# Kernel optimization log

Measured on AMD Instinct MI355X. Metric: run time of the kernel, lower is better.

Reference implementation:

```python
import jax, jax.numpy as jnp
import numpy as np

N = 50000   # nodes
E = 600000  # directed edges
B = 128     # graphs
IN = 128
H = 128
K = 30      # sort-pool k
C_OUT = 32
KER = 5
OUT_DIM = 10
L_OUT = K - KER + 1  # 26


def setup_inputs() -> dict:
    key = jax.random.key(0)
    ks = jax.random.split(key, 12)
    s = 0.05
    return {
        "x": jax.random.normal(ks[0], (N, IN), jnp.float32),
        "edge_index": jax.random.randint(ks[1], (2, E), 0, N),
        "batch": jnp.sort(jax.random.randint(ks[2], (N,), 0, B)),
        "W0": jax.random.normal(ks[3], (IN, H), jnp.float32) * s,
        "b0": jnp.zeros((H,), jnp.float32),
        "W1": jax.random.normal(ks[4], (H, H), jnp.float32) * s,
        "b1": jnp.zeros((H,), jnp.float32),
        "W2": jax.random.normal(ks[5], (H, H), jnp.float32) * s,
        "b2": jnp.zeros((H,), jnp.float32),
        "conv_w": jax.random.normal(ks[6], (C_OUT, H, KER), jnp.float32) * s,
        "conv_b": jnp.zeros((C_OUT,), jnp.float32),
        "lin1_w": jax.random.normal(ks[7], (C_OUT * L_OUT, H), jnp.float32) * s,
        "lin1_b": jnp.zeros((H,), jnp.float32),
        "lin2_w": jax.random.normal(ks[8], (H, OUT_DIM), jnp.float32) * s,
        "lin2_b": jnp.zeros((OUT_DIM,), jnp.float32),
    }


def reference(x, edge_index, batch, W0, b0, W1, b1, W2, b2,
              conv_w, conv_b, lin1_w, lin1_b, lin2_w, lin2_b):
    # --- GCN normalization (A + I, symmetric deg^-1/2) ---
    loops = jnp.arange(N)
    row = jnp.concatenate([edge_index[0], loops])  # source
    col = jnp.concatenate([edge_index[1], loops])  # target (aggregation side)
    deg = jax.ops.segment_sum(jnp.ones_like(col, dtype=x.dtype), col, num_segments=N)
    dinv = jax.lax.rsqrt(jnp.maximum(deg, 1.0))
    norm = dinv[row] * dinv[col]  # [E+N]

    def gcn(h, W, b):
        hw = h @ W                                            # [N,H]
        msg = hw[row] * norm[:, None]                         # gather [E+N,H]
        return jax.ops.segment_sum(msg, col, num_segments=N) + b

    h = jax.nn.relu(gcn(x, W0, b0))
    h = jax.nn.relu(gcn(h, W1, b1))
    h = jax.nn.relu(gcn(h, W2, b2))

    # --- SortAggregation: per-graph sort by last channel (desc), top-K, zero-pad ---
    last = h[:, -1]
    order = jnp.lexsort((-last, batch))  # primary: batch, secondary: last desc
    hs = h[order]
    bs = batch[order]
    counts = jax.ops.segment_sum(jnp.ones((N,), jnp.int32), batch, num_segments=B)
    starts = jnp.cumsum(counts) - counts  # exclusive prefix sum
    rank = jnp.arange(N) - starts[bs]     # within-graph rank after sort
    r = jnp.where(rank < K, rank, K)      # overflow bucket K is discarded
    pooled = jnp.zeros((B, K + 1, H), h.dtype).at[bs, r].add(hs)[:, :K]  # [B,K,H]

    # --- conv1d head (NCH layout, matches torch view/transpose) ---
    xc = jnp.transpose(pooled, (0, 2, 1))  # [B,H,K]
    y = jax.lax.conv_general_dilated(xc, conv_w, (1,), "VALID",
                                     dimension_numbers=("NCH", "OIH", "NCH"))
    y = jax.nn.relu(y + conv_b[None, :, None])  # [B,C_OUT,L_OUT]
    y = y.reshape(B, -1)
    y = jax.nn.relu(y @ lin1_w + lin1_b)
    return y @ lin2_w + lin2_b  # [B,OUT_DIM]
```

## Files before the change

### kernel.cpp

```cpp
#include <hip/hip_runtime.h>
#include <math.h>

#define Nn 50000
#define Ee 600000
#define Bg 128
#define Hd 128
#define Kt 30
#define CO 32
#define KW 5
#define LOUT 26
#define CAP 2048
#define SCB 196
#define MMB 782

typedef float v2f __attribute__((ext_vector_type(2)));
typedef short bf16x8 __attribute__((ext_vector_type(8)));
typedef float f32x4 __attribute__((ext_vector_type(4)));

__device__ __forceinline__ unsigned short bfr(float v) {
    unsigned u = __builtin_bit_cast(unsigned, v);
    unsigned r = (u + 0x7FFFu + ((u >> 16) & 1u)) >> 16;
    return (unsigned short)r;
}
__device__ __forceinline__ float bff(unsigned short h) {
    unsigned u = ((unsigned)h) << 16;
    return __builtin_bit_cast(float, u);
}

__global__ void countpack_kernel(const int* __restrict__ ei, const int* __restrict__ batch,
                            int* __restrict__ deg_i, int* __restrict__ bstart,
                            const float* __restrict__ conv_w, float* __restrict__ wT2,
                            const float* __restrict__ W0, const float* __restrict__ W1,
                            const float* __restrict__ W2,
                            ushort* __restrict__ Bph, ushort* __restrict__ Bpm,
                            ushort* __restrict__ Bpl) {
    int i = blockIdx.x * 256 + threadIdx.x;
    if (i < Ee) atomicAdd(&deg_i[ei[Ee + i]], 1);
    if (i < Nn) {
        int b = batch[i];
        if (i == 0) bstart[b] = 0;
        else if (batch[i - 1] != b) bstart[b] = i;
    }
    if (i == 0) bstart[Bg] = Nn;
    if (i < CO * KW * Hd) {
        int ci = i & 127;
        int r = i >> 7;
        int o = r / KW, k = r - o * KW;
        wT2[i] = conv_w[((size_t)o * Hd + ci) * KW + k];
    }
    if (i < 3 * 2048) {
        int l = i >> 11;
        int r = i & 2047;
        int kc = r >> 9;
        int n = (r >> 6) & 7;
        int lane = r & 63;
        int m = lane & 15, kq = lane >> 4;
        const float* W = (l == 0) ? W0 : (l == 1) ? W1 : W2;
        int col = n * 16 + m;
        size_t off = ((size_t)l * 2048 + (size_t)((kc * 8 + n) * 64 + lane)) * 8;
#pragma unroll
        for (int j = 0; j < 8; ++j) {
            float v = W[(size_t)(kc * 32 + kq * 8 + j) * Hd + col];
            unsigned short h = bfr(v);
            float r1 = v - bff(h);
            unsigned short mid = bfr(r1);
            Bph[off + j] = h;
            Bpm[off + j] = mid;
            Bpl[off + j] = bfr(r1 - bff(mid));
        }
    }
}

__global__ __launch_bounds__(256) void scanBC2_kernel(const int* __restrict__ deg_i,
                            int* __restrict__ row_ptr, float* __restrict__ dinv,
                            int* __restrict__ bstart) {
    __shared__ int ls[256];
    __shared__ int boffS;
    int tid = threadIdx.x;
    int b = blockIdx.x;
    int s = 0;
    for (int k = 0; k < b; ++k)
        s += deg_i[k * 256 + tid] + 1;
    ls[tid] = s;
    __syncthreads();
    for (int off = 128; off > 0; off >>= 1) {
        if (tid < off) ls[tid] += ls[tid + off];
        __syncthreads();
    }
    if (tid == 0) boffS = ls[0];
    __syncthreads();
    int boff = boffS;
    int i = b * 256 + tid;
    int v2 = 0;
    if (i < Nn) {
        int raw = deg_i[i];
        v2 = raw + 1;
        dinv[i] = 1.0f / sqrtf((float)(raw + 2));
    }
    ls[tid] = v2;
    __syncthreads();
    for (int off = 1; off < 256; off <<= 1) {
        int t = (tid >= off) ? ls[tid - off] : 0;
        __syncthreads();
        ls[tid] += t;
        __syncthreads();
    }
    if (i < Nn) row_ptr[i + 1] = ls[tid] + boff;
    if (i == 0) row_ptr[0] = 0;
    if (b == 0 && tid == 0) {
        for (int bb = Bg - 1; bb >= 0; --bb)
            if (bstart[bb] == -1) bstart[bb] = bstart[bb + 1];
    }
}

__device__ __forceinline__ void mmx_body(int bid, int tid,
                            const float* __restrict__ Hin,
                            const ushort* __restrict__ Bph, const ushort* __restrict__ Bpm,
                            const ushort* __restrict__ Bpl,
                            const float* __restrict__ dinv, float* __restrict__ hw,
                            float* __restrict__ col127) {
    __shared__ __align__(16) float At[64][132];
    int w = tid >> 6, lane = tid & 63;
    int m = lane & 15, kq = lane >> 4;
    {
        const f32x4* g4 = (const f32x4*)(Hin + (size_t)bid * 64 * Hd);
        int rowsLeft = Nn - bid * 64;
#pragma unroll
        for (int i = 0; i < 8; ++i) {
            int f = i * 256 + tid;
            int r = f >> 5, c4 = f & 31;
            f32x4 v = (f32x4)0.f;
            if (r < rowsLeft) v = g4[f];
            *(f32x4*)&At[r][c4 * 4] = v;
        }
    }
    __syncthreads();
    const float* arow = &At[w * 16 + m][0];
    f32x4 acc[8];
#pragma unroll
    for (int n = 0; n < 8; ++n) acc[n] = (f32x4)0.f;
#pragma unroll
    for (int kc = 0; kc < 4; ++kc) {
        bf16x8 a0, a1, a2;
        float av[8];
        *(f32x4*)&av[0] = *(const f32x4*)(arow + kc * 32 + kq * 8);
        *(f32x4*)&av[4] = *(const f32x4*)(arow + kc * 32 + kq * 8 + 4);
#pragma unroll
        for (int j = 0; j < 8; ++j) {
            unsigned short h = bfr(av[j]);
            float r1 = av[j] - bff(h);
            unsigned short mid = bfr(r1);
            a0[j] = (short)h;
            a1[j] = (short)mid;
            a2[j] = (short)bfr(r1 - bff(mid));
        }
        const ushort* bhp = Bph + (size_t)((kc * 8) * 64 + lane) * 8;
        const ushort* bmp = Bpm + (size_t)((kc * 8) * 64 + lane) * 8;
        const ushort* blp = Bpl + (size_t)((kc * 8) * 64 + lane) * 8;
#pragma unroll
        for (int n = 0; n < 8; ++n) {
            bf16x8 b0 = *(const bf16x8*)(bhp + (size_t)n * 64 * 8);
            bf16x8 b1 = *(const bf16x8*)(bmp + (size_t)n * 64 * 8);
            bf16x8 b2 = *(const bf16x8*)(blp + (size_t)n * 64 * 8);
            acc[n] = __builtin_amdgcn_mfma_f32_16x16x32_bf16(a0, b0, acc[n], 0, 0, 0);
            acc[n] = __builtin_amdgcn_mfma_f32_16x16x32_bf16(a1, b0, acc[n], 0, 0, 0);
            acc[n] = __builtin_amdgcn_mfma_f32_16x16x32_bf16(a0, b1, acc[n], 0, 0, 0);
            acc[n] = __builtin_amdgcn_mfma_f32_16x16x32_bf16(a1, b1, acc[n], 0, 0, 0);
            acc[n] = __builtin_amdgcn_mfma_f32_16x16x32_bf16(a2, b0, acc[n], 0, 0, 0);
            acc[n] = __builtin_amdgcn_mfma_f32_16x16x32_bf16(a0, b2, acc[n], 0, 0, 0);
        }
    }
    int rbase = bid * 64 + w * 16 + kq * 4;
#pragma unroll
    for (int reg = 0; reg < 4; ++reg) {
        int r = rbase + reg;
        if (r < Nn) {
            float s = dinv[r];
#pragma unroll
            for (int n = 0; n < 8; ++n)
                hw[(size_t)r * Hd + n * 16 + m] = acc[n][reg] * s;
            if (m == 15) col127[r] = acc[7][reg] * s;
        }
    }
}

__global__ __launch_bounds__(256) void mmx_kernel(const float* __restrict__ Hin,
                            const ushort* __restrict__ Bph, const ushort* __restrict__ Bpm,
                            const ushort* __restrict__ Bpl,
                            const float* __restrict__ dinv, float* __restrict__ hw,
                            float* __restrict__ col127) {
    mmx_body(blockIdx.x, threadIdx.x, Hin, Bph, Bpm, Bpl, dinv, hw, col127);
}

__global__ __launch_bounds__(256) void mmxfill_kernel(const float* __restrict__ Hin,
                            const ushort* __restrict__ Bph, const ushort* __restrict__ Bpm,
                            const ushort* __restrict__ Bpl,
                            const float* __restrict__ dinv, float* __restrict__ hw,
                            float* __restrict__ col127,
                            const int* __restrict__ ei, const int* __restrict__ row_ptr,
                            int* __restrict__ cnt, int* __restrict__ csr_src) {
    if (blockIdx.x < MMB) {
        mmx_body(blockIdx.x, threadIdx.x, Hin, Bph, Bpm, Bpl, dinv, hw, col127);
    } else {
        int e = (blockIdx.x - MMB) * 256 + threadIdx.x;
        if (e < Ee) {
            int c = ei[Ee + e];
            int r = ei[e];
            int p = row_ptr[c] + atomicAdd(&cnt[c], 1) + 1;
            csr_src[p] = r;
        }
    }
}

__global__ __launch_bounds__(256) void agg_kernel(const float* __restrict__ hw,
                            const int* __restrict__ row_ptr, const int* __restrict__ csr_src,
                            const float* __restrict__ dinv, const float* __restrict__ bias,
                            float* __restrict__ hout) {
    int node = blockIdx.x * 4 + (threadIdx.x >> 6);
    if (node >= Nn) return;
    int lane = threadIdx.x & 63;
    const v2f* hw2 = (const v2f*)hw;
    v2f a0 = hw2[(size_t)node * 64 + lane];
    v2f a1 = 0.f, a2 = 0.f, a3 = 0.f;
    v2f a4 = 0.f, a5 = 0.f, a6 = 0.f, a7 = 0.f;
    int e0 = row_ptr[node], e1 = row_ptr[node + 1];
    int e = e0;
    for (; e + 7 < e1; e += 8) {
        int s0 = __builtin_nontemporal_load(csr_src + e);
        int s1 = __builtin_nontemporal_load(csr_src + e + 1);
        int s2 = __builtin_nontemporal_load(csr_src + e + 2);
        int s3 = __builtin_nontemporal_load(csr_src + e + 3);
        int s4 = __builtin_nontemporal_load(csr_src + e + 4);
        int s5 = __builtin_nontemporal_load(csr_src + e + 5);
        int s6 = __builtin_nontemporal_load(csr_src + e + 6);
        int s7 = __builtin_nontemporal_load(csr_src + e + 7);
        a0 += hw2[(size_t)s0 * 64 + lane];
        a1 += hw2[(size_t)s1 * 64 + lane];
        a2 += hw2[(size_t)s2 * 64 + lane];
        a3 += hw2[(size_t)s3 * 64 + lane];
        a4 += hw2[(size_t)s4 * 64 + lane];
        a5 += hw2[(size_t)s5 * 64 + lane];
        a6 += hw2[(size_t)s6 * 64 + lane];
        a7 += hw2[(size_t)s7 * 64 + lane];
    }
    if (e + 3 < e1) {
        int s0 = __builtin_nontemporal_load(csr_src + e);
        int s1 = __builtin_nontemporal_load(csr_src + e + 1);
        int s2 = __builtin_nontemporal_load(csr_src + e + 2);
        int s3 = __builtin_nontemporal_load(csr_src + e + 3);
        a4 += hw2[(size_t)s0 * 64 + lane];
        a5 += hw2[(size_t)s1 * 64 + lane];
        a6 += hw2[(size_t)s2 * 64 + lane];
        a7 += hw2[(size_t)s3 * 64 + lane];
        e += 4;
    }
    for (; e < e1; ++e) {
        int s0 = __builtin_nontemporal_load(csr_src + e);
        a0 += hw2[(size_t)s0 * 64 + lane];
    }
    v2f acc = ((a0 + a1) + (a2 + a3)) + ((a4 + a5) + (a6 + a7));
    float d = dinv[node];
    v2f bv = ((const v2f*)bias)[lane];
    v2f o;
    o.x = fmaxf(fmaf(d, acc.x, bv.x), 0.f);
    o.y = fmaxf(fmaf(d, acc.y, bv.y), 0.f);
    ((v2f*)hout)[(size_t)node * 64 + lane] = o;
}

__global__ __launch_bounds__(1024) void tail_kernel(const float* __restrict__ hw,
                            const float* __restrict__ hw127,
                            const int* __restrict__ bstart, const int* __restrict__ row_ptr,
                            const int* __restrict__ csr_src, const float* __restrict__ dinv,
                            const float* __restrict__ b2,
                            const float* __restrict__ wT2, const float* __restrict__ conv_b,
                            const float* __restrict__ l1w, const float* __restrict__ l1b,
                            const float* __restrict__ l2w, const float* __restrict__ l2b,
                            float* __restrict__ out) {
    __shared__ float vals[CAP];
    __shared__ float xcl[Kt][130];
    __shared__ float fl[CO * LOUT];
    __shared__ float pz[8][Hd];
    __shared__ float z[Hd];
    __shared__ int selS[Kt];
    int b = blockIdx.x, tid = threadIdx.x;

    int s0 = bstart[b], s1 = bstart[b + 1];
    int n = s1 - s0;
    int nc = n < CAP ? n : CAP;
    if (tid < Kt) selS[tid] = -1;
    float b2l = b2[127];
    for (int j = tid; j < nc; j += 1024) {
        int node = s0 + j;
        float a0 = hw127[node];
        float a1 = 0.f, a2 = 0.f, a3 = 0.f, a4 = 0.f, a5 = 0.f, a6 = 0.f, a7 = 0.f;
        int e0 = row_ptr[node], e1 = row_ptr[node + 1];
        int e = e0;
        for (; e + 7 < e1; e += 8) {
            int q0 = __builtin_nontemporal_load(csr_src + e);
            int q1 = __builtin_nontemporal_load(csr_src + e + 1);
            int q2 = __builtin_nontemporal_load(csr_src + e + 2);
            int q3 = __builtin_nontemporal_load(csr_src + e + 3);
            int q4 = __builtin_nontemporal_load(csr_src + e + 4);
            int q5 = __builtin_nontemporal_load(csr_src + e + 5);
            int q6 = __builtin_nontemporal_load(csr_src + e + 6);
            int q7 = __builtin_nontemporal_load(csr_src + e + 7);
            a0 += hw127[q0];
            a1 += hw127[q1];
            a2 += hw127[q2];
            a3 += hw127[q3];
            a4 += hw127[q4];
            a5 += hw127[q5];
            a6 += hw127[q6];
            a7 += hw127[q7];
        }
        if (e + 3 < e1) {
            int q0 = __builtin_nontemporal_load(csr_src + e);
            int q1 = __builtin_nontemporal_load(csr_src + e + 1);
            int q2 = __builtin_nontemporal_load(csr_src + e + 2);
            int q3 = __builtin_nontemporal_load(csr_src + e + 3);
            a4 += hw127[q0];
            a5 += hw127[q1];
            a6 += hw127[q2];
            a7 += hw127[q3];
            e += 4;
        }
        for (; e < e1; ++e) {
            int q0 = __builtin_nontemporal_load(csr_src + e);
            a0 += hw127[q0];
        }
        float acc = ((a0 + a1) + (a2 + a3)) + ((a4 + a5) + (a6 + a7));
        vals[j] = fmaxf(fmaf(dinv[node], acc, b2l), 0.f);
    }
    __syncthreads();

    for (int j = tid; j < nc; j += 1024) {
        float vj = vals[j];
        int rank = 0;
        for (int i = 0; i < nc; ++i) {
            float vi = vals[i];
            rank += (vi > vj || (vi == vj && i < j)) ? 1 : 0;
        }
        if (rank < Kt) selS[rank] = s0 + j;
    }
    __syncthreads();

    int wv = tid >> 6, lane = tid & 63;
    const v2f* hw2 = (const v2f*)hw;
    v2f bv = ((const v2f*)b2)[lane];
    for (int t = wv; t < Kt; t += 16) {
        int s = selS[t];
        v2f o = (v2f)0.f;
        if (s >= 0) {
            v2f a0 = hw2[(size_t)s * 64 + lane];
            v2f a1 = 0.f, a2 = 0.f, a3 = 0.f;
            v2f a4 = 0.f, a5 = 0.f, a6 = 0.f, a7 = 0.f;
            int e0 = row_ptr[s], e1 = row_ptr[s + 1];
            int e = e0;
            for (; e + 7 < e1; e += 8) {
                int q0 = __builtin_nontemporal_load(csr_src + e);
                int q1 = __builtin_nontemporal_load(csr_src + e + 1);
                int q2 = __builtin_nontemporal_load(csr_src + e + 2);
                int q3 = __builtin_nontemporal_load(csr_src + e + 3);
                int q4 = __builtin_nontemporal_load(csr_src + e + 4);
                int q5 = __builtin_nontemporal_load(csr_src + e + 5);
                int q6 = __builtin_nontemporal_load(csr_src + e + 6);
                int q7 = __builtin_nontemporal_load(csr_src + e + 7);
                a0 += hw2[(size_t)q0 * 64 + lane];
                a1 += hw2[(size_t)q1 * 64 + lane];
                a2 += hw2[(size_t)q2 * 64 + lane];
                a3 += hw2[(size_t)q3 * 64 + lane];
                a4 += hw2[(size_t)q4 * 64 + lane];
                a5 += hw2[(size_t)q5 * 64 + lane];
                a6 += hw2[(size_t)q6 * 64 + lane];
                a7 += hw2[(size_t)q7 * 64 + lane];
            }
            if (e + 3 < e1) {
                int q0 = __builtin_nontemporal_load(csr_src + e);
                int q1 = __builtin_nontemporal_load(csr_src + e + 1);
                int q2 = __builtin_nontemporal_load(csr_src + e + 2);
                int q3 = __builtin_nontemporal_load(csr_src + e + 3);
                a4 += hw2[(size_t)q0 * 64 + lane];
                a5 += hw2[(size_t)q1 * 64 + lane];
                a6 += hw2[(size_t)q2 * 64 + lane];
                a7 += hw2[(size_t)q3 * 64 + lane];
                e += 4;
            }
            for (; e < e1; ++e) {
                int q0 = __builtin_nontemporal_load(csr_src + e);
                a0 += hw2[(size_t)q0 * 64 + lane];
            }
            v2f acc = ((a0 + a1) + (a2 + a3)) + ((a4 + a5) + (a6 + a7));
            float d = dinv[s];
            o.x = fmaxf(fmaf(d, acc.x, bv.x), 0.f);
            o.y = fmaxf(fmaf(d, acc.y, bv.y), 0.f);
        }
        xcl[t][lane * 2] = o.x;
        xcl[t][lane * 2 + 1] = o.y;
    }
    __syncthreads();
    if (tid < CO * LOUT) {
        int o = tid / LOUT, t = tid - o * LOUT;
        float acc = conv_b[o];
#pragma unroll
        for (int k = 0; k < KW; ++k) {
            const float* xr = &xcl[t + k][0];
            const float* wr = wT2 + ((size_t)o * KW + k) * Hd;
#pragma unroll 8
            for (int c4 = 0; c4 < 32; ++c4) {
                float2 xa = *(const float2*)(xr + c4 * 4);
                float2 xb = *(const float2*)(xr + c4 * 4 + 2);
                float4 wv2 = *(const float4*)(wr + c4 * 4);
                acc = fmaf(xa.x, wv2.x, acc);
                acc = fmaf(xa.y, wv2.y, acc);
                acc = fmaf(xb.x, wv2.z, acc);
                acc = fmaf(xb.y, wv2.w, acc);
            }
        }
        fl[tid] = fmaxf(acc, 0.f);
    }
    __syncthreads();
    int hh = tid & 127, chunk = tid >> 7;
    int m0 = chunk * 104;
    float acc = 0.f;
    const float* lw = l1w + (size_t)m0 * Hd + hh;
#pragma unroll 8
    for (int m = 0; m < 104; ++m)
        acc = fmaf(fl[m0 + m], lw[(size_t)m * Hd], acc);
    pz[chunk][hh] = acc;
    __syncthreads();
    if (tid < Hd) {
        float a = l1b[tid];
#pragma unroll
        for (int q = 0; q < 8; ++q) a += pz[q][tid];
        z[tid] = fmaxf(a, 0.f);
    }
    __syncthreads();
    if (tid < 10) {
        float a2 = l2b[tid];
        for (int j = 0; j < Hd; ++j)
            a2 = fmaf(z[j], l2w[j * 10 + tid], a2);
        out[b * 10 + tid] = a2;
    }
}

extern "C" void kernel_launch(void* const* d_in, const int* in_sizes, int n_in,
                              void* d_out, int out_size, void* d_ws, size_t ws_size,
                              hipStream_t stream) {
    const float* x      = (const float*)d_in[0];
    const int*   ei     = (const int*)d_in[1];
    const int*   batch  = (const int*)d_in[2];
    const float* W0     = (const float*)d_in[3];
    const float* b0     = (const float*)d_in[4];
    const float* W1     = (const float*)d_in[5];
    const float* b1     = (const float*)d_in[6];
    const float* W2     = (const float*)d_in[7];
    const float* b2     = (const float*)d_in[8];
    const float* conv_w = (const float*)d_in[9];
    const float* conv_b = (const float*)d_in[10];
    const float* l1w    = (const float*)d_in[11];
    const float* l1b    = (const float*)d_in[12];
    const float* l2w    = (const float*)d_in[13];
    const float* l2b    = (const float*)d_in[14];
    float* out = (float*)d_out;

    int* wsI = (int*)d_ws;
    size_t off = 0;
    int*   deg_i   = wsI + off; off += Nn;
    int*   cnt     = wsI + off; off += Nn;
    int*   bstart  = wsI + off; off += 132;
    int*   row_ptr = wsI + off; off += 50004;
    float* dinv    = (float*)(wsI + off); off += Nn;
    int*   csr_src = wsI + off; off += Ee;
    off = (off + 3) & ~(size_t)3;
    ushort* Bph  = (ushort*)(wsI + off); off += 3 * 16384 / 2;
    ushort* Bpm  = (ushort*)(wsI + off); off += 3 * 16384 / 2;
    ushort* Bpl  = (ushort*)(wsI + off); off += 3 * 16384 / 2;
    float* hw    = (float*)(wsI + off); off += (size_t)Nn * Hd;
    float* hbuf  = (float*)(wsI + off); off += (size_t)Nn * Hd;
    float* wT2   = (float*)(wsI + off); off += CO * KW * Hd;
    float* hw127 = (float*)(wsI + off); off += Nn;

    hipMemsetAsync(deg_i, 0xFF, (size_t)(Nn + Nn + 132) * 4, stream);
    countpack_kernel<<<(Ee + 255) / 256, 256, 0, stream>>>(ei, batch, deg_i, bstart,
        conv_w, wT2, W0, W1, W2, Bph, Bpm, Bpl);
    scanBC2_kernel<<<SCB, 256, 0, stream>>>(deg_i, row_ptr, dinv, bstart);
    dim3 aggGrid((Nn + 3) / 4);
    mmxfill_kernel<<<MMB + (Ee + 255) / 256, 256, 0, stream>>>(x, Bph, Bpm, Bpl,
        dinv, hw, hw127, ei, row_ptr, cnt, csr_src);
    agg_kernel<<<aggGrid, 256, 0, stream>>>(hw, row_ptr, csr_src, dinv, b0, hbuf);
    mmx_kernel<<<MMB, 256, 0, stream>>>(hbuf, Bph + 16384, Bpm + 16384, Bpl + 16384,
        dinv, hw, hw127);
    agg_kernel<<<aggGrid, 256, 0, stream>>>(hw, row_ptr, csr_src, dinv, b1, hbuf);
    mmx_kernel<<<MMB, 256, 0, stream>>>(hbuf, Bph + 32768, Bpm + 32768, Bpl + 32768,
        dinv, hw, hw127);
    tail_kernel<<<Bg, 1024, 0, stream>>>(hw, hw127, bstart, row_ptr, csr_src, dinv, b2,
                                         wT2, conv_b, l1w, l1b, l2w, l2b, out);
}
```

Before: 393.4 us.

## Fuse GCN aggregation with next layer's MFMA matmul in one kernel

Merges the neighbour aggregation of layers 0 and 1 with the following layer's feature transform into one 1024-thread kernel. Each block aggregates 64 nodes into shared memory, then runs the split-bf16 MFMA matmul on that tile. This drops the intermediate hbuf round trip through global memory and two kernel launches. The cost is a larger block with a barrier between the gather and MFMA phases, which may lower occupancy and overlap. The buffers are now ping-ponged between hw and hbuf so a kernel never reads and writes the same array.

```diff
diff --git a/kernel.cpp b/kernel.cpp
--- a/kernel.cpp
+++ b/kernel.cpp
@@ -117,8 +117,7 @@
                             const float* __restrict__ Hin,
                             const ushort* __restrict__ Bph, const ushort* __restrict__ Bpm,
                             const ushort* __restrict__ Bpl,
-                            const float* __restrict__ dinv, float* __restrict__ hw,
-                            float* __restrict__ col127) {
+                            const float* __restrict__ dinv, float* __restrict__ hw) {
     __shared__ __align__(16) float At[64][132];
     int w = tid >> 6, lane = tid & 63;
     int m = lane & 15, kq = lane >> 4;
@@ -179,28 +178,18 @@
 #pragma unroll
             for (int n = 0; n < 8; ++n)
                 hw[(size_t)r * Hd + n * 16 + m] = acc[n][reg] * s;
-            if (m == 15) col127[r] = acc[7][reg] * s;
-        }
-    }
-}
-
-__global__ __launch_bounds__(256) void mmx_kernel(const float* __restrict__ Hin,
-                            const ushort* __restrict__ Bph, const ushort* __restrict__ Bpm,
-                            const ushort* __restrict__ Bpl,
-                            const float* __restrict__ dinv, float* __restrict__ hw,
-                            float* __restrict__ col127) {
-    mmx_body(blockIdx.x, threadIdx.x, Hin, Bph, Bpm, Bpl, dinv, hw, col127);
+        }
+    }
 }
 
 __global__ __launch_bounds__(256) void mmxfill_kernel(const float* __restrict__ Hin,
                             const ushort* __restrict__ Bph, const ushort* __restrict__ Bpm,
                             const ushort* __restrict__ Bpl,
                             const float* __restrict__ dinv, float* __restrict__ hw,
-                            float* __restrict__ col127,
                             const int* __restrict__ ei, const int* __restrict__ row_ptr,
                             int* __restrict__ cnt, int* __restrict__ csr_src) {
     if (blockIdx.x < MMB) {
-        mmx_body(blockIdx.x, threadIdx.x, Hin, Bph, Bpm, Bpl, dinv, hw, col127);
+        mmx_body(blockIdx.x, threadIdx.x, Hin, Bph, Bpm, Bpl, dinv, hw);
     } else {
         int e = (blockIdx.x - MMB) * 256 + threadIdx.x;
         if (e < Ee) {
@@ -212,59 +201,126 @@
     }
 }
 
-__global__ __launch_bounds__(256) void agg_kernel(const float* __restrict__ hw,
+__global__ __launch_bounds__(1024, 8) void aggmm_kernel(const float* __restrict__ hwin,
                             const int* __restrict__ row_ptr, const int* __restrict__ csr_src,
                             const float* __restrict__ dinv, const float* __restrict__ bias,
-                            float* __restrict__ hout) {
-    int node = blockIdx.x * 4 + (threadIdx.x >> 6);
-    if (node >= Nn) return;
-    int lane = threadIdx.x & 63;
-    const v2f* hw2 = (const v2f*)hw;
-    v2f a0 = hw2[(size_t)node * 64 + lane];
-    v2f a1 = 0.f, a2 = 0.f, a3 = 0.f;
-    v2f a4 = 0.f, a5 = 0.f, a6 = 0.f, a7 = 0.f;
-    int e0 = row_ptr[node], e1 = row_ptr[node + 1];
-    int e = e0;
-    for (; e + 7 < e1; e += 8) {
-        int s0 = __builtin_nontemporal_load(csr_src + e);
-        int s1 = __builtin_nontemporal_load(csr_src + e + 1);
-        int s2 = __builtin_nontemporal_load(csr_src + e + 2);
-        int s3 = __builtin_nontemporal_load(csr_src + e + 3);
-        int s4 = __builtin_nontemporal_load(csr_src + e + 4);
-        int s5 = __builtin_nontemporal_load(csr_src + e + 5);
-        int s6 = __builtin_nontemporal_load(csr_src + e + 6);
-        int s7 = __builtin_nontemporal_load(csr_src + e + 7);
-        a0 += hw2[(size_t)s0 * 64 + lane];
-        a1 += hw2[(size_t)s1 * 64 + lane];
-        a2 += hw2[(size_t)s2 * 64 + lane];
-        a3 += hw2[(size_t)s3 * 64 + lane];
-        a4 += hw2[(size_t)s4 * 64 + lane];
-        a5 += hw2[(size_t)s5 * 64 + lane];
-        a6 += hw2[(size_t)s6 * 64 + lane];
-        a7 += hw2[(size_t)s7 * 64 + lane];
-    }
-    if (e + 3 < e1) {
-        int s0 = __builtin_nontemporal_load(csr_src + e);
-        int s1 = __builtin_nontemporal_load(csr_src + e + 1);
-        int s2 = __builtin_nontemporal_load(csr_src + e + 2);
-        int s3 = __builtin_nontemporal_load(csr_src + e + 3);
-        a4 += hw2[(size_t)s0 * 64 + lane];
-        a5 += hw2[(size_t)s1 * 64 + lane];
-        a6 += hw2[(size_t)s2 * 64 + lane];
-        a7 += hw2[(size_t)s3 * 64 + lane];
-        e += 4;
-    }
-    for (; e < e1; ++e) {
-        int s0 = __builtin_nontemporal_load(csr_src + e);
-        a0 += hw2[(size_t)s0 * 64 + lane];
-    }
-    v2f acc = ((a0 + a1) + (a2 + a3)) + ((a4 + a5) + (a6 + a7));
-    float d = dinv[node];
+                            const ushort* __restrict__ Bph, const ushort* __restrict__ Bpm,
+                            const ushort* __restrict__ Bpl,
+                            float* __restrict__ hwout, float* __restrict__ col127) {
+    __shared__ __align__(16) float At[64][132];
+    int tid = threadIdx.x;
+    int w = tid >> 6, lane = tid & 63;
+    int bid = blockIdx.x;
+    const v2f* hw2 = (const v2f*)hwin;
     v2f bv = ((const v2f*)bias)[lane];
-    v2f o;
-    o.x = fmaxf(fmaf(d, acc.x, bv.x), 0.f);
-    o.y = fmaxf(fmaf(d, acc.y, bv.y), 0.f);
-    ((v2f*)hout)[(size_t)node * 64 + lane] = o;
+#pragma unroll
+    for (int t = 0; t < 4; ++t) {
+        int rl = w * 4 + t;
+        int node = bid * 64 + rl;
+        v2f o = (v2f)0.f;
+        if (node < Nn) {
+            v2f a0 = hw2[(size_t)node * 64 + lane];
+            v2f a1 = 0.f, a2 = 0.f, a3 = 0.f;
+            v2f a4 = 0.f, a5 = 0.f, a6 = 0.f, a7 = 0.f;
+            int e0 = row_ptr[node], e1 = row_ptr[node + 1];
+            int e = e0;
+            for (; e + 7 < e1; e += 8) {
+                int s0 = __builtin_nontemporal_load(csr_src + e);
+                int s1 = __builtin_nontemporal_load(csr_src + e + 1);
+                int s2 = __builtin_nontemporal_load(csr_src + e + 2);
+                int s3 = __builtin_nontemporal_load(csr_src + e + 3);
+                int s4 = __builtin_nontemporal_load(csr_src + e + 4);
+                int s5 = __builtin_nontemporal_load(csr_src + e + 5);
+                int s6 = __builtin_nontemporal_load(csr_src + e + 6);
+                int s7 = __builtin_nontemporal_load(csr_src + e + 7);
+                a0 += hw2[(size_t)s0 * 64 + lane];
+                a1 += hw2[(size_t)s1 * 64 + lane];
+                a2 += hw2[(size_t)s2 * 64 + lane];
+                a3 += hw2[(size_t)s3 * 64 + lane];
+                a4 += hw2[(size_t)s4 * 64 + lane];
+                a5 += hw2[(size_t)s5 * 64 + lane];
+                a6 += hw2[(size_t)s6 * 64 + lane];
+                a7 += hw2[(size_t)s7 * 64 + lane];
+            }
+            if (e + 3 < e1) {
+                int s0 = __builtin_nontemporal_load(csr_src + e);
+                int s1 = __builtin_nontemporal_load(csr_src + e + 1);
+                int s2 = __builtin_nontemporal_load(csr_src + e + 2);
+                int s3 = __builtin_nontemporal_load(csr_src + e + 3);
+                a4 += hw2[(size_t)s0 * 64 + lane];
+                a5 += hw2[(size_t)s1 * 64 + lane];
+                a6 += hw2[(size_t)s2 * 64 + lane];
+                a7 += hw2[(size_t)s3 * 64 + lane];
+                e += 4;
+            }
+            for (; e < e1; ++e) {
+                int s0 = __builtin_nontemporal_load(csr_src + e);
+                a0 += hw2[(size_t)s0 * 64 + lane];
+            }
+            v2f acc = ((a0 + a1) + (a2 + a3)) + ((a4 + a5) + (a6 + a7));
+            float d = dinv[node];
+            o.x = fmaxf(fmaf(d, acc.x, bv.x), 0.f);
+            o.y = fmaxf(fmaf(d, acc.y, bv.y), 0.f);
+        }
+        *(v2f*)&At[rl][lane * 2] = o;
+    }
+    __syncthreads();
+    int g = w >> 2, n0 = (w & 3) * 2;
+    int m = lane & 15, kq = lane >> 4;
+    const float* arow = &At[g * 16 + m][0];
+    f32x4 acc0 = (f32x4)0.f, acc1 = (f32x4)0.f;
+#pragma unroll
+    for (int kc = 0; kc < 4; ++kc) {
+        bf16x8 a0, a1, a2;
+        float av[8];
+        *(f32x4*)&av[0] = *(const f32x4*)(arow + kc * 32 + kq * 8);
+        *(f32x4*)&av[4] = *(const f32x4*)(arow + kc * 32 + kq * 8 + 4);
+#pragma unroll
+        for (int j = 0; j < 8; ++j) {
+            unsigned short h = bfr(av[j]);
+            float r1 = av[j] - bff(h);
+            unsigned short mid = bfr(r1);
+            a0[j] = (short)h;
+            a1[j] = (short)mid;
+            a2[j] = (short)bfr(r1 - bff(mid));
+        }
+        const ushort* bhp = Bph + (size_t)((kc * 8 + n0) * 64 + lane) * 8;
+        const ushort* bmp = Bpm + (size_t)((kc * 8 + n0) * 64 + lane) * 8;
+        const ushort* blp = Bpl + (size_t)((kc * 8 + n0) * 64 + lane) * 8;
+        {
+            bf16x8 b0 = *(const bf16x8*)bhp;
+            bf16x8 b1 = *(const bf16x8*)bmp;
+            bf16x8 b2 = *(const bf16x8*)blp;
+            acc0 = __builtin_amdgcn_mfma_f32_16x16x32_bf16(a0, b0, acc0, 0, 0, 0);
+            acc0 = __builtin_amdgcn_mfma_f32_16x16x32_bf16(a1, b0, acc0, 0, 0, 0);
+            acc0 = __builtin_amdgcn_mfma_f32_16x16x32_bf16(a0, b1, acc0, 0, 0, 0);
+            acc0 = __builtin_amdgcn_mfma_f32_16x16x32_bf16(a1, b1, acc0, 0, 0, 0);
+            acc0 = __builtin_amdgcn_mfma_f32_16x16x32_bf16(a2, b0, acc0, 0, 0, 0);
+            acc0 = __builtin_amdgcn_mfma_f32_16x16x32_bf16(a0, b2, acc0, 0, 0, 0);
+        }
+        {
+            bf16x8 b0 = *(const bf16x8*)(bhp + 64 * 8);
+            bf16x8 b1 = *(const bf16x8*)(bmp + 64 * 8);
+            bf16x8 b2 = *(const bf16x8*)(blp + 64 * 8);
+            acc1 = __builtin_amdgcn_mfma_f32_16x16x32_bf16(a0, b0, acc1, 0, 0, 0);
+            acc1 = __builtin_amdgcn_mfma_f32_16x16x32_bf16(a1, b0, acc1, 0, 0, 0);
+            acc1 = __builtin_amdgcn_mfma_f32_16x16x32_bf16(a0, b1, acc1, 0, 0, 0);
+            acc1 = __builtin_amdgcn_mfma_f32_16x16x32_bf16(a1, b1, acc1, 0, 0, 0);
+            acc1 = __builtin_amdgcn_mfma_f32_16x16x32_bf16(a2, b0, acc1, 0, 0, 0);
+            acc1 = __builtin_amdgcn_mfma_f32_16x16x32_bf16(a0, b2, acc1, 0, 0, 0);
+        }
+    }
+    int rbase = bid * 64 + g * 16 + kq * 4;
+#pragma unroll
+    for (int reg = 0; reg < 4; ++reg) {
+        int r = rbase + reg;
+        if (r < Nn) {
+            float s = dinv[r];
+            hwout[(size_t)r * Hd + n0 * 16 + m] = acc0[reg] * s;
+            hwout[(size_t)r * Hd + (n0 + 1) * 16 + m] = acc1[reg] * s;
+            if (n0 == 6 && m == 15) col127[r] = acc1[reg] * s;
+        }
+    }
 }
 
 __global__ __launch_bounds__(1024) void tail_kernel(const float* __restrict__ hw,
@@ -484,15 +540,12 @@
     countpack_kernel<<<(Ee + 255) / 256, 256, 0, stream>>>(ei, batch, deg_i, bstart,
         conv_w, wT2, W0, W1, W2, Bph, Bpm, Bpl);
     scanBC2_kernel<<<SCB, 256, 0, stream>>>(deg_i, row_ptr, dinv, bstart);
-    dim3 aggGrid((Nn + 3) / 4);
     mmxfill_kernel<<<MMB + (Ee + 255) / 256, 256, 0, stream>>>(x, Bph, Bpm, Bpl,
-        dinv, hw, hw127, ei, row_ptr, cnt, csr_src);
-    agg_kernel<<<aggGrid, 256, 0, stream>>>(hw, row_ptr, csr_src, dinv, b0, hbuf);
-    mmx_kernel<<<MMB, 256, 0, stream>>>(hbuf, Bph + 16384, Bpm + 16384, Bpl + 16384,
-        dinv, hw, hw127);
-    agg_kernel<<<aggGrid, 256, 0, stream>>>(hw, row_ptr, csr_src, dinv, b1, hbuf);
-    mmx_kernel<<<MMB, 256, 0, stream>>>(hbuf, Bph + 32768, Bpm + 32768, Bpl + 32768,
-        dinv, hw, hw127);
+        dinv, hw, ei, row_ptr, cnt, csr_src);
+    aggmm_kernel<<<MMB, 1024, 0, stream>>>(hw, row_ptr, csr_src, dinv, b0,
+        Bph + 16384, Bpm + 16384, Bpl + 16384, hbuf, hw127);
+    aggmm_kernel<<<MMB, 1024, 0, stream>>>(hbuf, row_ptr, csr_src, dinv, b1,
+        Bph + 32768, Bpm + 32768, Bpl + 32768, hw, hw127);
     tail_kernel<<<Bg, 1024, 0, stream>>>(hw, hw127, bstart, row_ptr, csr_src, dinv, b2,
                                          wT2, conv_b, l1w, l1b, l2w, l2b, out);
 }
```

New measurement: 394.6 us. No clear change (+0.3%).
